# Kernel tuning notes

Hardware: AMD Instinct MI355X
Metric: run time of the kernel (lower is better)

The kernel has to match this reference:

```python
import jax, jax.numpy as jnp
import numpy as np

N_NODES = 50000
N_EDGES = 1600000
D_IN = 128
D_HID = 128
D_OUT = 3
EPS = 1e-5


def setup_inputs() -> dict:
    key = jax.random.key(0)
    ks = jax.random.split(key, 16)
    def lin(k, fi, fo):
        s = 1.0 / np.sqrt(fi)
        return jax.random.uniform(k, (fi, fo), jnp.float32, -s, s)
    inp = {
        "x": jax.random.normal(ks[0], (N_NODES, D_IN), jnp.float32),
        "edge_index": jax.random.randint(ks[1], (2, N_EDGES), 0, N_NODES, jnp.int32),
        "W1": lin(ks[2], D_IN, D_HID), "b1": jnp.zeros((D_HID,), jnp.float32),
        "W2": lin(ks[3], D_HID, D_HID), "b2": jnp.zeros((D_HID,), jnp.float32),
        "W3": lin(ks[4], D_HID, D_HID), "b3": jnp.zeros((D_HID,), jnp.float32),
        "g1": jnp.ones((D_HID,), jnp.float32), "beta1": jnp.zeros((D_HID,), jnp.float32),
        "g2": jnp.ones((D_HID,), jnp.float32), "beta2": jnp.zeros((D_HID,), jnp.float32),
        "Wp1": lin(ks[5], D_HID, D_HID), "bp1": jnp.zeros((D_HID,), jnp.float32),
        "Wp2": lin(ks[6], D_HID, D_OUT), "bp2": jnp.zeros((D_OUT,), jnp.float32),
    }
    return inp


def _gcn_norm(edge_index, n):
    # add self-loops, symmetric normalization (PyG GCNConv default)
    loops = jnp.arange(n, dtype=edge_index.dtype)
    row = jnp.concatenate([edge_index[0], loops])  # source
    col = jnp.concatenate([edge_index[1], loops])  # target
    deg = jax.ops.segment_sum(jnp.ones_like(col, jnp.float32), col, num_segments=n)
    dinv = jnp.where(deg > 0, jax.lax.rsqrt(deg), 0.0)
    norm = dinv[row] * dinv[col]  # [E+N]
    return row, col, norm


def _gcn_conv(x, W, b, row, col, norm, n):
    h = x @ W                                # [N, F]
    msg = h[row] * norm[:, None]             # [E+N, F] gather
    out = jax.ops.segment_sum(msg, col, num_segments=n)  # scatter-add
    return out + b


def _layernorm(x, g, beta):
    mu = jnp.mean(x, axis=-1, keepdims=True)
    var = jnp.var(x, axis=-1, keepdims=True)
    return (x - mu) * jax.lax.rsqrt(var + EPS) * g + beta


def reference(x, edge_index, W1, b1, W2, b2, W3, b3, g1, beta1, g2, beta2, Wp1, bp1, Wp2, bp2):
    n = x.shape[0]
    row, col, norm = _gcn_norm(edge_index, n)
    # layer 0
    h = _gcn_conv(x, W1, b1, row, col, norm, n)
    h = _layernorm(jax.nn.relu(h), g1, beta1)  # dropout = identity (eval mode)
    # layer 1
    h = _gcn_conv(h, W2, b2, row, col, norm, n)
    h = _layernorm(jax.nn.relu(h), g2, beta2)
    # layer 2 (no layernorm)
    h = _gcn_conv(h, W3, b3, row, col, norm, n)
    h = jax.nn.relu(h)
    # post-MP MLP head (dropout = identity in eval)
    h = h @ Wp1 + bp1
    return h @ Wp2 + bp2
```

## Files before the change

kernel.cpp:

```cpp
#include <hip/hip_runtime.h>
#include <hip/hip_bf16.h>

#define EPS_LN 1e-5f
#define NB    256
#define SEGCAP 16384

typedef int ivec4 __attribute__((ext_vector_type(4)));
typedef short bf16x8v __attribute__((ext_vector_type(8)));
typedef float f32x4v __attribute__((ext_vector_type(4)));


__global__ __launch_bounds__(256) void bucket_hist(const int* __restrict__ col,
                                                   int* __restrict__ chunkBH,
                                                   int E, int per, int nbuck) {
    __shared__ int hist[256];
    int t = threadIdx.x;
    hist[t] = 0;
    __syncthreads();
    int s0 = blockIdx.x * per;
    int s1 = s0 + per; if (s1 > E) s1 = E;
    if (s0 < s1) {
        int q0 = s0 >> 2, q1 = s1 >> 2;
        for (int i = q0 + t; i < q1; i += 256) {
            ivec4 c = __builtin_nontemporal_load((const ivec4*)col + i);
            atomicAdd(&hist[c.x >> 8], 1);
            atomicAdd(&hist[c.y >> 8], 1);
            atomicAdd(&hist[c.z >> 8], 1);
            atomicAdd(&hist[c.w >> 8], 1);
        }
        for (int i = (q1 << 2) + t; i < s1; i += 256)
            atomicAdd(&hist[col[i] >> 8], 1);
    }
    __syncthreads();
    if (t < nbuck) chunkBH[blockIdx.x * 256 + t] = hist[t];
}

__global__ __launch_bounds__(256) void bucket_scan(int* __restrict__ chunkBH,
                                                   int* __restrict__ bucketStart,
                                                   int* __restrict__ rowPtr,
                                                   int E, int n, int nbuck, int nb) {
    __shared__ int tot[256];
    int t = threadIdx.x;
    int run = 0;
    if (t < nbuck) {
        for (int k0 = 0; k0 < nb; k0 += 16) {
            int v[16];
#pragma unroll
            for (int j = 0; j < 16; j++)
                v[j] = (k0 + j < nb) ? chunkBH[(k0 + j) * 256 + t] : 0;
#pragma unroll
            for (int j = 0; j < 16; j++) {
                int tv = v[j];
                if (k0 + j < nb) chunkBH[(k0 + j) * 256 + t] = run;
                run += tv;
            }
        }
    }
    tot[t] = run;
    __syncthreads();
    for (int d = 1; d < 256; d <<= 1) {
        int add = (t >= d) ? tot[t - d] : 0;
        __syncthreads();
        tot[t] += add;
        __syncthreads();
    }
    if (t < nbuck) bucketStart[t] = tot[t] - run;
    if (t == 0) { bucketStart[nbuck] = E; rowPtr[n] = E; }
}

__global__ __launch_bounds__(256) void scatter_pairs(const int* __restrict__ row,
                                                     const int* __restrict__ col,
                                                     const int* __restrict__ chunkBH,
                                                     const int* __restrict__ bucketStart,
                                                     unsigned long long* __restrict__ tmp,
                                                     int E, int per, int nbuck) {
    __shared__ int curs[256];
    int t = threadIdx.x;
    int k = blockIdx.x;
    curs[t] = (t < nbuck) ? (chunkBH[k * 256 + t] + bucketStart[t]) : 0;
    __syncthreads();
    int s0 = k * per;
    int s1 = s0 + per; if (s1 > E) s1 = E;
    if (s0 >= s1) return;
    int q0 = s0 >> 2, q1 = s1 >> 2;
    for (int i = q0 + t; i < q1; i += 256) {
        ivec4 c4 = __builtin_nontemporal_load((const ivec4*)col + i);
        ivec4 r4 = __builtin_nontemporal_load((const ivec4*)row + i);
        int p0 = atomicAdd(&curs[c4.x >> 8], 1);
        tmp[p0] = ((unsigned long long)(unsigned)c4.x << 32) | (unsigned)r4.x;
        int p1 = atomicAdd(&curs[c4.y >> 8], 1);
        tmp[p1] = ((unsigned long long)(unsigned)c4.y << 32) | (unsigned)r4.y;
        int p2 = atomicAdd(&curs[c4.z >> 8], 1);
        tmp[p2] = ((unsigned long long)(unsigned)c4.z << 32) | (unsigned)r4.z;
        int p3 = atomicAdd(&curs[c4.w >> 8], 1);
        tmp[p3] = ((unsigned long long)(unsigned)c4.w << 32) | (unsigned)r4.w;
    }
    for (int i = (q1 << 2) + t; i < s1; i += 256) {
        int c = col[i], r = row[i];
        int p = atomicAdd(&curs[c >> 8], 1);
        tmp[p] = ((unsigned long long)(unsigned)c << 32) | (unsigned)r;
    }
}

__global__ __launch_bounds__(256) void bucket_fill(const unsigned long long* __restrict__ tmp,
                                                   const int* __restrict__ bucketStart,
                                                   int* __restrict__ rowPtr,
                                                   float* __restrict__ dinv,
                                                   int* __restrict__ srcList,
                                                   int n) {
    __shared__ int cnt[256];
    __shared__ int cur[256];
    __shared__ int seg[SEGCAP];
    int b = blockIdx.x, t = threadIdx.x;
    int node0 = b << 8;
    int s0 = bucketStart[b], s1 = bucketStart[b + 1];
    int len = s1 - s0;
    cnt[t] = 0;
    __syncthreads();
    for (int i = s0 + t; i < s1; i += 256) {
        int c = (int)(tmp[i] >> 32);
        atomicAdd(&cnt[c - node0], 1);
    }
    __syncthreads();
    int v = cnt[t];
    cur[t] = v;
    __syncthreads();
    for (int d = 1; d < 256; d <<= 1) {
        int add = (t >= d) ? cur[t - d] : 0;
        __syncthreads();
        cur[t] += add;
        __syncthreads();
    }
    int excl = cur[t] - v;
    int node = node0 + t;
    if (node < n) {
        rowPtr[node] = s0 + excl;
        dinv[node] = rsqrtf((float)v + 1.0f);
    }
    cur[t] = excl;
    __syncthreads();
    if (len <= SEGCAP) {
        for (int i = s0 + t; i < s1; i += 256) {
            unsigned long long p = tmp[i];
            int c = (int)(p >> 32);
            int r = (int)(p & 0xffffffffu);
            int pos = atomicAdd(&cur[c - node0], 1);
            seg[pos] = r;
        }
        __syncthreads();
        for (int i = t; i < len; i += 256)
            srcList[s0 + i] = seg[i];
    } else {
        for (int i = s0 + t; i < s1; i += 256) {
            unsigned long long p = tmp[i];
            int c = (int)(p >> 32);
            int r = (int)(p & 0xffffffffu);
            int pos = atomicAdd(&cur[c - node0], 1);
            srcList[s0 + pos] = r;
        }
    }
}

__global__ __launch_bounds__(256) void pack_w(const float* __restrict__ W,
                                              unsigned short* __restrict__ Wp) {
    int t = threadIdx.x;
    for (int s = t; s < 16384; s += 256) {
        int i = s & 7;
        int lane = (s >> 3) & 63;
        int jt = (s >> 9) & 7;
        int kb = s >> 12;
        int k = kb * 32 + ((lane >> 4) & 3) * 8 + i;
        int nn = jt * 16 + (lane & 15);
        float v = W[k * 128 + nn];
        __hip_bfloat16 hi = __float2bfloat16(v);
        float hf = __bfloat162float(hi);
        __hip_bfloat16 lo = __float2bfloat16(v - hf);
        Wp[s]         = *(unsigned short*)&hi;
        Wp[16384 + s] = *(unsigned short*)&lo;
    }
}

__global__ __launch_bounds__(256) void cast_hilo(const float* __restrict__ x,
                                                 unsigned short* __restrict__ hi,
                                                 unsigned short* __restrict__ lo,
                                                 int total4) {
    int i = blockIdx.x * 256 + threadIdx.x;
    if (i >= total4) return;
    float4 v = ((const float4*)x)[i];
    ushort4 h, l;
    __hip_bfloat16 b;
    float f;
    b = __float2bfloat16(v.x); f = __bfloat162float(b); h.x = *(unsigned short*)&b;
    b = __float2bfloat16(v.x - f); l.x = *(unsigned short*)&b;
    b = __float2bfloat16(v.y); f = __bfloat162float(b); h.y = *(unsigned short*)&b;
    b = __float2bfloat16(v.y - f); l.y = *(unsigned short*)&b;
    b = __float2bfloat16(v.z); f = __bfloat162float(b); h.z = *(unsigned short*)&b;
    b = __float2bfloat16(v.z - f); l.z = *(unsigned short*)&b;
    b = __float2bfloat16(v.w); f = __bfloat162float(b); h.w = *(unsigned short*)&b;
    b = __float2bfloat16(v.w - f); l.w = *(unsigned short*)&b;
    ((ushort4*)hi)[i] = h;
    ((ushort4*)lo)[i] = l;
}

__global__ __launch_bounds__(256) void gemm_mfma(const unsigned short* __restrict__ Ahi,
                                                 const unsigned short* __restrict__ Alo,
                                                 const unsigned short* __restrict__ Wp,
                                                 const float* __restrict__ dinv,
                                                 unsigned short* __restrict__ hbOut,
                                                 int n) {
    const int tx = threadIdx.x;
    const int wv = tx >> 6;
    const int l  = tx & 63;
    const int m0 = blockIdx.x * 64 + wv * 16;
    int arow = m0 + (l & 15);
    if (arow >= n) arow = 0;
    const int kofs = (l >> 4) * 8;

    f32x4v acc[8];
#pragma unroll
    for (int jt = 0; jt < 8; jt++) acc[jt] = (f32x4v){0.f, 0.f, 0.f, 0.f};

#pragma unroll
    for (int kb = 0; kb < 4; kb++) {
        bf16x8v ah = *(const bf16x8v*)(Ahi + (size_t)arow * 128 + kb * 32 + kofs);
        bf16x8v al = *(const bf16x8v*)(Alo + (size_t)arow * 128 + kb * 32 + kofs);
        const unsigned short* wb = Wp + (kb * 8) * 512 + l * 8;
#pragma unroll
        for (int jt = 0; jt < 8; jt++) {
            bf16x8v bh = *(const bf16x8v*)(wb + jt * 512);
            bf16x8v bl = *(const bf16x8v*)(wb + jt * 512 + 16384);
            acc[jt] = __builtin_amdgcn_mfma_f32_16x16x32_bf16(ah, bh, acc[jt], 0, 0, 0);
            acc[jt] = __builtin_amdgcn_mfma_f32_16x16x32_bf16(ah, bl, acc[jt], 0, 0, 0);
            acc[jt] = __builtin_amdgcn_mfma_f32_16x16x32_bf16(al, bh, acc[jt], 0, 0, 0);
        }
    }

    const int r0 = m0 + (l >> 4) * 4;
    const int colb = l & 15;
#pragma unroll
    for (int r = 0; r < 4; r++) {
        int grow = r0 + r;
        if (grow < n) {
            float dv = dinv[grow];
#pragma unroll
            for (int jt = 0; jt < 8; jt++) {
                __hip_bfloat16 t = __float2bfloat16(acc[jt][r] * dv);
                hbOut[(size_t)grow * 128 + jt * 16 + colb] = *(unsigned short*)&t;
            }
        }
    }
}

#define BF_LO(u) __uint_as_float((u) << 16)
#define BF_HI(u) __uint_as_float((u) & 0xffff0000u)

__global__ __launch_bounds__(128) void agg_post(const unsigned int* __restrict__ hb,
                                                const int* __restrict__ rowPtr,
                                                const int* __restrict__ srcList,
                                                const float* __restrict__ dinv,
                                                const float* __restrict__ b,
                                                const float* __restrict__ g,
                                                const float* __restrict__ beta,
                                                unsigned short* __restrict__ outHi,
                                                unsigned short* __restrict__ outLo,
                                                int n) {
    int wid = (blockIdx.x * 128 + threadIdx.x) >> 6;
    int lane = threadIdx.x & 63;
    if (wid >= n) return;
    int h = lane & 15;
    int gg = lane >> 4;
    int e0 = rowPtr[wid], e1 = rowPtr[wid + 1];
    float dc = dinv[wid];
    const uint4* hb4 = (const uint4*)hb;

    uint4 us = hb4[(size_t)wid * 16 + h];

    float a[8];
#pragma unroll
    for (int j = 0; j < 8; j++) a[j] = 0.f;

    int idx0 = (e0 + gg < e1) ? srcList[e0 + gg] : -1;
    int idx1 = (e0 + 4 + gg < e1) ? srcList[e0 + 4 + gg] : -1;
    int e = e0;
    for (; e + 8 <= e1; e += 8) {
        int ni0 = (e + 8 + gg < e1) ? srcList[e + 8 + gg] : -1;
        int ni1 = (e + 12 + gg < e1) ? srcList[e + 12 + gg] : -1;
        uint4 u0 = hb4[(size_t)idx0 * 16 + h];
        uint4 u1 = hb4[(size_t)idx1 * 16 + h];
        a[0] += BF_LO(u0.x); a[1] += BF_HI(u0.x);
        a[2] += BF_LO(u0.y); a[3] += BF_HI(u0.y);
        a[4] += BF_LO(u0.z); a[5] += BF_HI(u0.z);
        a[6] += BF_LO(u0.w); a[7] += BF_HI(u0.w);
        a[0] += BF_LO(u1.x); a[1] += BF_HI(u1.x);
        a[2] += BF_LO(u1.y); a[3] += BF_HI(u1.y);
        a[4] += BF_LO(u1.z); a[5] += BF_HI(u1.z);
        a[6] += BF_LO(u1.w); a[7] += BF_HI(u1.w);
        idx0 = ni0; idx1 = ni1;
    }
    if (idx0 >= 0) {
        uint4 u = hb4[(size_t)idx0 * 16 + h];
        a[0] += BF_LO(u.x); a[1] += BF_HI(u.x);
        a[2] += BF_LO(u.y); a[3] += BF_HI(u.y);
        a[4] += BF_LO(u.z); a[5] += BF_HI(u.z);
        a[6] += BF_LO(u.w); a[7] += BF_HI(u.w);
    }
    if (idx1 >= 0) {
        uint4 u = hb4[(size_t)idx1 * 16 + h];
        a[0] += BF_LO(u.x); a[1] += BF_HI(u.x);
        a[2] += BF_LO(u.y); a[3] += BF_HI(u.y);
        a[4] += BF_LO(u.z); a[5] += BF_HI(u.z);
        a[6] += BF_LO(u.w); a[7] += BF_HI(u.w);
    }
#pragma unroll
    for (int j = 0; j < 8; j++) {
        a[j] += __shfl_xor(a[j], 16, 64);
        a[j] += __shfl_xor(a[j], 32, 64);
    }
    a[0] += BF_LO(us.x); a[1] += BF_HI(us.x);
    a[2] += BF_LO(us.y); a[3] += BF_HI(us.y);
    a[4] += BF_LO(us.z); a[5] += BF_HI(us.z);
    a[6] += BF_LO(us.w); a[7] += BF_HI(us.w);

    float4 bv0 = *(const float4*)(b + h * 8);
    float4 bv1 = *(const float4*)(b + h * 8 + 4);
    a[0] = fmaxf(a[0] * dc + bv0.x, 0.f);
    a[1] = fmaxf(a[1] * dc + bv0.y, 0.f);
    a[2] = fmaxf(a[2] * dc + bv0.z, 0.f);
    a[3] = fmaxf(a[3] * dc + bv0.w, 0.f);
    a[4] = fmaxf(a[4] * dc + bv1.x, 0.f);
    a[5] = fmaxf(a[5] * dc + bv1.y, 0.f);
    a[6] = fmaxf(a[6] * dc + bv1.z, 0.f);
    a[7] = fmaxf(a[7] * dc + bv1.w, 0.f);

    float s = ((a[0] + a[1]) + (a[2] + a[3])) + ((a[4] + a[5]) + (a[6] + a[7]));
#pragma unroll
    for (int m = 8; m >= 1; m >>= 1) s += __shfl_xor(s, m, 64);
    float mu = s * (1.f / 128.f);
    float sq = 0.f;
    float d[8];
#pragma unroll
    for (int j = 0; j < 8; j++) { d[j] = a[j] - mu; sq += d[j] * d[j]; }
#pragma unroll
    for (int m = 8; m >= 1; m >>= 1) sq += __shfl_xor(sq, m, 64);
    float rs = rsqrtf(sq * (1.f / 128.f) + EPS_LN);
    float4 gv0 = *(const float4*)(g + h * 8);
    float4 gv1 = *(const float4*)(g + h * 8 + 4);
    float4 bt0 = *(const float4*)(beta + h * 8);
    float4 bt1 = *(const float4*)(beta + h * 8 + 4);
    a[0] = d[0] * rs * gv0.x + bt0.x;
    a[1] = d[1] * rs * gv0.y + bt0.y;
    a[2] = d[2] * rs * gv0.z + bt0.z;
    a[3] = d[3] * rs * gv0.w + bt0.w;
    a[4] = d[4] * rs * gv1.x + bt1.x;
    a[5] = d[5] * rs * gv1.y + bt1.y;
    a[6] = d[6] * rs * gv1.z + bt1.z;
    a[7] = d[7] * rs * gv1.w + bt1.w;

    if (gg == 0) {
        ushort4 h0, h1, l0, l1;
        __hip_bfloat16 bb; float ff;
        bb = __float2bfloat16(a[0]); ff = __bfloat162float(bb); h0.x = *(unsigned short*)&bb;
        bb = __float2bfloat16(a[0] - ff); l0.x = *(unsigned short*)&bb;
        bb = __float2bfloat16(a[1]); ff = __bfloat162float(bb); h0.y = *(unsigned short*)&bb;
        bb = __float2bfloat16(a[1] - ff); l0.y = *(unsigned short*)&bb;
        bb = __float2bfloat16(a[2]); ff = __bfloat162float(bb); h0.z = *(unsigned short*)&bb;
        bb = __float2bfloat16(a[2] - ff); l0.z = *(unsigned short*)&bb;
        bb = __float2bfloat16(a[3]); ff = __bfloat162float(bb); h0.w = *(unsigned short*)&bb;
        bb = __float2bfloat16(a[3] - ff); l0.w = *(unsigned short*)&bb;
        bb = __float2bfloat16(a[4]); ff = __bfloat162float(bb); h1.x = *(unsigned short*)&bb;
        bb = __float2bfloat16(a[4] - ff); l1.x = *(unsigned short*)&bb;
        bb = __float2bfloat16(a[5]); ff = __bfloat162float(bb); h1.y = *(unsigned short*)&bb;
        bb = __float2bfloat16(a[5] - ff); l1.y = *(unsigned short*)&bb;
        bb = __float2bfloat16(a[6]); ff = __bfloat162float(bb); h1.z = *(unsigned short*)&bb;
        bb = __float2bfloat16(a[6] - ff); l1.z = *(unsigned short*)&bb;
        bb = __float2bfloat16(a[7]); ff = __bfloat162float(bb); h1.w = *(unsigned short*)&bb;
        bb = __float2bfloat16(a[7] - ff); l1.w = *(unsigned short*)&bb;
        size_t base = (size_t)wid * 128 + h * 8;
        *(ushort4*)(outHi + base)     = h0;
        *(ushort4*)(outHi + base + 4) = h1;
        *(ushort4*)(outLo + base)     = l0;
        *(ushort4*)(outLo + base + 4) = l1;
    }
}

__global__ __launch_bounds__(128) void agg_head(
        const unsigned int* __restrict__ hb,
        const int* __restrict__ rowPtr,
        const int* __restrict__ srcList,
        const float* __restrict__ dinv,
        const float* __restrict__ b,
        const float* __restrict__ Weff,
        const float* __restrict__ beff,
        float* __restrict__ out, int n) {
    __shared__ float Wl[384];
    int tt = threadIdx.x;
    Wl[tt] = Weff[tt]; Wl[tt + 128] = Weff[tt + 128]; Wl[tt + 256] = Weff[tt + 256];
    __syncthreads();

    int wid = (blockIdx.x * 128 + tt) >> 6;
    int lane = tt & 63;
    if (wid >= n) return;
    int h = lane & 15;
    int gg = lane >> 4;
    int e0 = rowPtr[wid], e1 = rowPtr[wid + 1];
    float dc = dinv[wid];
    const uint4* hb4 = (const uint4*)hb;
    uint4 us = hb4[(size_t)wid * 16 + h];

    float a[8];
#pragma unroll
    for (int j = 0; j < 8; j++) a[j] = 0.f;

    int idx0 = (e0 + gg < e1) ? srcList[e0 + gg] : -1;
    int idx1 = (e0 + 4 + gg < e1) ? srcList[e0 + 4 + gg] : -1;
    int e = e0;
    for (; e + 8 <= e1; e += 8) {
        int ni0 = (e + 8 + gg < e1) ? srcList[e + 8 + gg] : -1;
        int ni1 = (e + 12 + gg < e1) ? srcList[e + 12 + gg] : -1;
        uint4 u0 = hb4[(size_t)idx0 * 16 + h];
        uint4 u1 = hb4[(size_t)idx1 * 16 + h];
        a[0] += BF_LO(u0.x); a[1] += BF_HI(u0.x);
        a[2] += BF_LO(u0.y); a[3] += BF_HI(u0.y);
        a[4] += BF_LO(u0.z); a[5] += BF_HI(u0.z);
        a[6] += BF_LO(u0.w); a[7] += BF_HI(u0.w);
        a[0] += BF_LO(u1.x); a[1] += BF_HI(u1.x);
        a[2] += BF_LO(u1.y); a[3] += BF_HI(u1.y);
        a[4] += BF_LO(u1.z); a[5] += BF_HI(u1.z);
        a[6] += BF_LO(u1.w); a[7] += BF_HI(u1.w);
        idx0 = ni0; idx1 = ni1;
    }
    if (idx0 >= 0) {
        uint4 u = hb4[(size_t)idx0 * 16 + h];
        a[0] += BF_LO(u.x); a[1] += BF_HI(u.x);
        a[2] += BF_LO(u.y); a[3] += BF_HI(u.y);
        a[4] += BF_LO(u.z); a[5] += BF_HI(u.z);
        a[6] += BF_LO(u.w); a[7] += BF_HI(u.w);
    }
    if (idx1 >= 0) {
        uint4 u = hb4[(size_t)idx1 * 16 + h];
        a[0] += BF_LO(u.x); a[1] += BF_HI(u.x);
        a[2] += BF_LO(u.y); a[3] += BF_HI(u.y);
        a[4] += BF_LO(u.z); a[5] += BF_HI(u.z);
        a[6] += BF_LO(u.w); a[7] += BF_HI(u.w);
    }
#pragma unroll
    for (int j = 0; j < 8; j++) {
        a[j] += __shfl_xor(a[j], 16, 64);
        a[j] += __shfl_xor(a[j], 32, 64);
    }
    a[0] += BF_LO(us.x); a[1] += BF_HI(us.x);
    a[2] += BF_LO(us.y); a[3] += BF_HI(us.y);
    a[4] += BF_LO(us.z); a[5] += BF_HI(us.z);
    a[6] += BF_LO(us.w); a[7] += BF_HI(us.w);

    float4 bv0 = *(const float4*)(b + h * 8);
    float4 bv1 = *(const float4*)(b + h * 8 + 4);
    a[0] = fmaxf(a[0] * dc + bv0.x, 0.f);
    a[1] = fmaxf(a[1] * dc + bv0.y, 0.f);
    a[2] = fmaxf(a[2] * dc + bv0.z, 0.f);
    a[3] = fmaxf(a[3] * dc + bv0.w, 0.f);
    a[4] = fmaxf(a[4] * dc + bv1.x, 0.f);
    a[5] = fmaxf(a[5] * dc + bv1.y, 0.f);
    a[6] = fmaxf(a[6] * dc + bv1.z, 0.f);
    a[7] = fmaxf(a[7] * dc + bv1.w, 0.f);

    float p0 = 0.f, p1 = 0.f, p2 = 0.f;
#pragma unroll
    for (int j = 0; j < 8; j++) {
        const float* w = &Wl[(8 * h + j) * 3];
        p0 += a[j] * w[0];
        p1 += a[j] * w[1];
        p2 += a[j] * w[2];
    }
#pragma unroll
    for (int m = 8; m >= 1; m >>= 1) {
        p0 += __shfl_xor(p0, m, 64);
        p1 += __shfl_xor(p1, m, 64);
        p2 += __shfl_xor(p2, m, 64);
    }
    if (lane == 0) {
        out[(size_t)wid * 3 + 0] = p0 + beff[0];
        out[(size_t)wid * 3 + 1] = p1 + beff[1];
        out[(size_t)wid * 3 + 2] = p2 + beff[2];
    }
}

__global__ __launch_bounds__(128) void head_collapse(const float* __restrict__ Wp1,
                                                     const float* __restrict__ bp1,
                                                     const float* __restrict__ Wp2,
                                                     const float* __restrict__ bp2,
                                                     float* __restrict__ Weff,
                                                     float* __restrict__ beff) {
    __shared__ float w2[384];
    int t = threadIdx.x;
    w2[t] = Wp2[t]; w2[t + 128] = Wp2[t + 128]; w2[t + 256] = Wp2[t + 256];
    __syncthreads();
    float p0 = 0.f, p1 = 0.f, p2 = 0.f;
    const float* wr = Wp1 + (size_t)t * 128;
    for (int k = 0; k < 128; k++) {
        float v = wr[k];
        p0 += v * w2[k * 3 + 0];
        p1 += v * w2[k * 3 + 1];
        p2 += v * w2[k * 3 + 2];
    }
    Weff[t * 3 + 0] = p0; Weff[t * 3 + 1] = p1; Weff[t * 3 + 2] = p2;
    if (t == 0) {
        float q0 = bp2[0], q1 = bp2[1], q2 = bp2[2];
        for (int k = 0; k < 128; k++) {
            float v = bp1[k];
            q0 += v * w2[k * 3 + 0];
            q1 += v * w2[k * 3 + 1];
            q2 += v * w2[k * 3 + 2];
        }
        beff[0] = q0; beff[1] = q1; beff[2] = q2;
    }
}

extern "C" void kernel_launch(void* const* d_in, const int* in_sizes, int n_in,
                              void* d_out, int out_size, void* d_ws, size_t ws_size,
                              hipStream_t stream) {
    const float* x   = (const float*)d_in[0];
    const int* ei    = (const int*)d_in[1];
    const float* W1  = (const float*)d_in[2];
    const float* b1  = (const float*)d_in[3];
    const float* W2  = (const float*)d_in[4];
    const float* b2  = (const float*)d_in[5];
    const float* W3  = (const float*)d_in[6];
    const float* b3  = (const float*)d_in[7];
    const float* g1  = (const float*)d_in[8];
    const float* be1 = (const float*)d_in[9];
    const float* g2  = (const float*)d_in[10];
    const float* be2 = (const float*)d_in[11];
    const float* Wp1f = (const float*)d_in[12];
    const float* bp1 = (const float*)d_in[13];
    const float* Wp2f = (const float*)d_in[14];
    const float* bp2 = (const float*)d_in[15];
    float* out = (float*)d_out;

    const int n = in_sizes[0] / 128;
    const int E = in_sizes[1] / 2;
    const int* row = ei;
    const int* col = ei + E;

    char* ws = (char*)d_ws;
    size_t nA  = ((size_t)n * 4 + 255) & ~(size_t)255;
    size_t nA1 = ((size_t)(n + 1) * 4 + 255) & ~(size_t)255;
    size_t eA  = ((size_t)E * 4 + 255) & ~(size_t)255;
    size_t hbSz = ((size_t)n * 128 * 2 + 255) & ~(size_t)255;
    int*   rowPtr  = (int*)ws;
    float* dinvp   = (float*)(ws + nA1);
    int*   srcList = (int*)(ws + nA1 + nA);
    unsigned short* hbA = (unsigned short*)(ws + nA1 + nA + eA);
    unsigned short* hbB = hbA + hbSz / 2;
    unsigned short* Phi = hbB + hbSz / 2;
    unsigned short* Plo = Phi + hbSz / 2;
    unsigned short* Wq1 = Plo + hbSz / 2;
    unsigned short* Wq2 = Wq1 + 32768;
    unsigned short* Wq3 = Wq2 + 32768;
    float* Weff = (float*)(Wq3 + 32768);
    float* beff = Weff + 384;
    unsigned long long* tmp = (unsigned long long*)Phi;
    int* chunkBH     = (int*)((char*)Phi + 2 * eA);
    int* bucketStart = (int*)((char*)Phi + 2 * eA + (size_t)NB * 256 * 4);

    const int nbuck = (n + 255) >> 8;
    const int per   = (((E + NB - 1) / NB) + 15) & ~15;
    const int tileBlocks = (n + 63) / 64;
    const int nodeWaveBlocks = (n + 1) / 2;
    const int castBlocks = (n * 128 / 4 + 255) / 256;

    bucket_hist<<<NB, 256, 0, stream>>>(col, chunkBH, E, per, nbuck);
    bucket_scan<<<1, 256, 0, stream>>>(chunkBH, bucketStart, rowPtr, E, n, nbuck, NB);
    scatter_pairs<<<NB, 256, 0, stream>>>(row, col, chunkBH, bucketStart, tmp, E, per, nbuck);
    bucket_fill<<<nbuck, 256, 0, stream>>>(tmp, bucketStart, rowPtr, dinvp, srcList, n);
    head_collapse<<<1, 128, 0, stream>>>(Wp1f, bp1, Wp2f, bp2, Weff, beff);
    pack_w<<<1, 256, 0, stream>>>(W1, Wq1);
    pack_w<<<1, 256, 0, stream>>>(W2, Wq2);
    pack_w<<<1, 256, 0, stream>>>(W3, Wq3);

    cast_hilo<<<castBlocks, 256, 0, stream>>>(x, Phi, Plo, n * 128 / 4);

    gemm_mfma<<<tileBlocks, 256, 0, stream>>>(Phi, Plo, Wq1, dinvp, hbA, n);
    agg_post<<<nodeWaveBlocks, 128, 0, stream>>>((const unsigned int*)hbA,
                                                 rowPtr, srcList, dinvp,
                                                 b1, g1, be1, Phi, Plo, n);
    gemm_mfma<<<tileBlocks, 256, 0, stream>>>(Phi, Plo, Wq2, dinvp, hbB, n);
    agg_post<<<nodeWaveBlocks, 128, 0, stream>>>((const unsigned int*)hbB,
                                                 rowPtr, srcList, dinvp,
                                                 b2, g2, be2, Phi, Plo, n);
    gemm_mfma<<<tileBlocks, 256, 0, stream>>>(Phi, Plo, Wq3, dinvp, hbA, n);
    agg_head<<<nodeWaveBlocks, 128, 0, stream>>>((const unsigned int*)hbA,
                                                 rowPtr, srcList, dinvp,
                                                 b3, Weff, beff, out, n);
}
```

Before: 414.3 us.

## Fuse input hi/lo split into GEMM, stage weights in LDS, merge weight packing

```diff
diff --git a/kernel.cpp b/kernel.cpp
--- a/kernel.cpp
+++ b/kernel.cpp
@@ -8,6 +8,7 @@
 typedef int ivec4 __attribute__((ext_vector_type(4)));
 typedef short bf16x8v __attribute__((ext_vector_type(8)));
 typedef float f32x4v __attribute__((ext_vector_type(4)));
+typedef unsigned short u16x8 __attribute__((ext_vector_type(8)));
 
 
 __global__ __launch_bounds__(256) void bucket_hist(const int* __restrict__ col,
@@ -161,53 +162,51 @@
     }
 }
 
-__global__ __launch_bounds__(256) void pack_w(const float* __restrict__ W,
-                                              unsigned short* __restrict__ Wp) {
-    int t = threadIdx.x;
-    for (int s = t; s < 16384; s += 256) {
-        int i = s & 7;
-        int lane = (s >> 3) & 63;
-        int jt = (s >> 9) & 7;
-        int kb = s >> 12;
-        int k = kb * 32 + ((lane >> 4) & 3) * 8 + i;
-        int nn = jt * 16 + (lane & 15);
-        float v = W[k * 128 + nn];
-        __hip_bfloat16 hi = __float2bfloat16(v);
-        float hf = __bfloat162float(hi);
-        __hip_bfloat16 lo = __float2bfloat16(v - hf);
-        Wp[s]         = *(unsigned short*)&hi;
-        Wp[16384 + s] = *(unsigned short*)&lo;
-    }
-}
-
-__global__ __launch_bounds__(256) void cast_hilo(const float* __restrict__ x,
-                                                 unsigned short* __restrict__ hi,
-                                                 unsigned short* __restrict__ lo,
-                                                 int total4) {
-    int i = blockIdx.x * 256 + threadIdx.x;
-    if (i >= total4) return;
-    float4 v = ((const float4*)x)[i];
-    ushort4 h, l;
-    __hip_bfloat16 b;
-    float f;
-    b = __float2bfloat16(v.x); f = __bfloat162float(b); h.x = *(unsigned short*)&b;
-    b = __float2bfloat16(v.x - f); l.x = *(unsigned short*)&b;
-    b = __float2bfloat16(v.y); f = __bfloat162float(b); h.y = *(unsigned short*)&b;
-    b = __float2bfloat16(v.y - f); l.y = *(unsigned short*)&b;
-    b = __float2bfloat16(v.z); f = __bfloat162float(b); h.z = *(unsigned short*)&b;
-    b = __float2bfloat16(v.z - f); l.z = *(unsigned short*)&b;
-    b = __float2bfloat16(v.w); f = __bfloat162float(b); h.w = *(unsigned short*)&b;
-    b = __float2bfloat16(v.w - f); l.w = *(unsigned short*)&b;
-    ((ushort4*)hi)[i] = h;
-    ((ushort4*)lo)[i] = l;
-}
-
-__global__ __launch_bounds__(256) void gemm_mfma(const unsigned short* __restrict__ Ahi,
+__global__ __launch_bounds__(256) void pack_w_all(const float* __restrict__ W1,
+                                                  const float* __restrict__ W2,
+                                                  const float* __restrict__ W3,
+                                                  unsigned short* __restrict__ Wq) {
+    int w = blockIdx.x >> 6;
+    const float* W = (w == 0) ? W1 : (w == 1) ? W2 : W3;
+    unsigned short* Wp = Wq + (size_t)w * 32768;
+    int s = (blockIdx.x & 63) * 256 + threadIdx.x;
+    int i = s & 7;
+    int lane = (s >> 3) & 63;
+    int jt = (s >> 9) & 7;
+    int kb = s >> 12;
+    int k = kb * 32 + ((lane >> 4) & 3) * 8 + i;
+    int nn = jt * 16 + (lane & 15);
+    float v = W[k * 128 + nn];
+    __hip_bfloat16 hi = __float2bfloat16(v);
+    float hf = __bfloat162float(hi);
+    __hip_bfloat16 lo = __float2bfloat16(v - hf);
+    Wp[s]         = *(unsigned short*)&hi;
+    Wp[16384 + s] = *(unsigned short*)&lo;
+}
+
+__device__ __forceinline__ void split8(const float* __restrict__ p,
+                                       bf16x8v& ah, bf16x8v& al) {
+#pragma unroll
+    for (int i = 0; i < 8; i++) {
+        float v = p[i];
+        __hip_bfloat16 hb = __float2bfloat16(v);
+        float hf = __bfloat162float(hb);
+        __hip_bfloat16 lb = __float2bfloat16(v - hf);
+        ah[i] = *(short*)&hb;
+        al[i] = *(short*)&lb;
+    }
+}
+
+template<int ASRC>
+__global__ __launch_bounds__(256) void gemm_mfma(const float* __restrict__ Af32,
+                                                 const unsigned short* __restrict__ Ahi,
                                                  const unsigned short* __restrict__ Alo,
                                                  const unsigned short* __restrict__ Wp,
                                                  const float* __restrict__ dinv,
                                                  unsigned short* __restrict__ hbOut,
                                                  int n) {
+    __shared__ unsigned short Bs[8192];
+
     const int tx = threadIdx.x;
     const int wv = tx >> 6;
     const int l  = tx & 63;
@@ -222,13 +221,27 @@
 
 #pragma unroll
     for (int kb = 0; kb < 4; kb++) {
-        bf16x8v ah = *(const bf16x8v*)(Ahi + (size_t)arow * 128 + kb * 32 + kofs);
-        bf16x8v al = *(const bf16x8v*)(Alo + (size_t)arow * 128 + kb * 32 + kofs);
-        const unsigned short* wb = Wp + (kb * 8) * 512 + l * 8;
+        __syncthreads();
+        {
+            u16x8* dH = (u16x8*)&Bs[tx * 16];
+            const u16x8* sH = (const u16x8*)(Wp + kb * 4096 + tx * 16);
+            dH[0] = sH[0]; dH[1] = sH[1];
+            u16x8* dL = (u16x8*)&Bs[4096 + tx * 16];
+            const u16x8* sL = (const u16x8*)(Wp + 16384 + kb * 4096 + tx * 16);
+            dL[0] = sL[0]; dL[1] = sL[1];
+        }
+        bf16x8v ah, al;
+        if (ASRC == 0) {
+            split8(Af32 + (size_t)arow * 128 + kb * 32 + kofs, ah, al);
+        } else {
+            ah = *(const bf16x8v*)(Ahi + (size_t)arow * 128 + kb * 32 + kofs);
+            al = *(const bf16x8v*)(Alo + (size_t)arow * 128 + kb * 32 + kofs);
+        }
+        __syncthreads();
 #pragma unroll
         for (int jt = 0; jt < 8; jt++) {
-            bf16x8v bh = *(const bf16x8v*)(wb + jt * 512);
-            bf16x8v bl = *(const bf16x8v*)(wb + jt * 512 + 16384);
+            bf16x8v bh = *(const bf16x8v*)&Bs[jt * 512 + l * 8];
+            bf16x8v bl = *(const bf16x8v*)&Bs[4096 + jt * 512 + l * 8];
             acc[jt] = __builtin_amdgcn_mfma_f32_16x16x32_bf16(ah, bh, acc[jt], 0, 0, 0);
             acc[jt] = __builtin_amdgcn_mfma_f32_16x16x32_bf16(ah, bl, acc[jt], 0, 0, 0);
             acc[jt] = __builtin_amdgcn_mfma_f32_16x16x32_bf16(al, bh, acc[jt], 0, 0, 0);
@@ -394,7 +407,11 @@
         float* __restrict__ out, int n) {
     __shared__ float Wl[384];
     int tt = threadIdx.x;
-    Wl[tt] = Weff[tt]; Wl[tt + 128] = Weff[tt + 128]; Wl[tt + 256] = Weff[tt + 256];
+    for (int idx = tt; idx < 384; idx += 128) {
+        int f = idx / 3, c = idx - f * 3;
+        int j = f & 7, hh = f >> 3;
+        Wl[(j * 3 + c) * 16 + hh] = Weff[idx];
+    }
     __syncthreads();
 
     int wid = (blockIdx.x * 128 + tt) >> 6;
@@ -467,10 +484,9 @@
     float p0 = 0.f, p1 = 0.f, p2 = 0.f;
 #pragma unroll
     for (int j = 0; j < 8; j++) {
-        const float* w = &Wl[(8 * h + j) * 3];
-        p0 += a[j] * w[0];
-        p1 += a[j] * w[1];
-        p2 += a[j] * w[2];
+        p0 += a[j] * Wl[(j * 3 + 0) * 16 + h];
+        p1 += a[j] * Wl[(j * 3 + 1) * 16 + h];
+        p2 += a[j] * Wl[(j * 3 + 2) * 16 + h];
     }
 #pragma unroll
     for (int m = 8; m >= 1; m >>= 1) {
@@ -554,10 +570,8 @@
     unsigned short* hbB = hbA + hbSz / 2;
     unsigned short* Phi = hbB + hbSz / 2;
     unsigned short* Plo = Phi + hbSz / 2;
-    unsigned short* Wq1 = Plo + hbSz / 2;
-    unsigned short* Wq2 = Wq1 + 32768;
-    unsigned short* Wq3 = Wq2 + 32768;
-    float* Weff = (float*)(Wq3 + 32768);
+    unsigned short* Wq  = Plo + hbSz / 2;
+    float* Weff = (float*)(Wq + 3 * 32768);
     float* beff = Weff + 384;
     unsigned long long* tmp = (unsigned long long*)Phi;
     int* chunkBH     = (int*)((char*)Phi + 2 * eA);
@@ -567,28 +581,23 @@
     const int per   = (((E + NB - 1) / NB) + 15) & ~15;
     const int tileBlocks = (n + 63) / 64;
     const int nodeWaveBlocks = (n + 1) / 2;
-    const int castBlocks = (n * 128 / 4 + 255) / 256;
 
     bucket_hist<<<NB, 256, 0, stream>>>(col, chunkBH, E, per, nbuck);
     bucket_scan<<<1, 256, 0, stream>>>(chunkBH, bucketStart, rowPtr, E, n, nbuck, NB);
     scatter_pairs<<<NB, 256, 0, stream>>>(row, col, chunkBH, bucketStart, tmp, E, per, nbuck);
     bucket_fill<<<nbuck, 256, 0, stream>>>(tmp, bucketStart, rowPtr, dinvp, srcList, n);
     head_collapse<<<1, 128, 0, stream>>>(Wp1f, bp1, Wp2f, bp2, Weff, beff);
-    pack_w<<<1, 256, 0, stream>>>(W1, Wq1);
-    pack_w<<<1, 256, 0, stream>>>(W2, Wq2);
-    pack_w<<<1, 256, 0, stream>>>(W3, Wq3);
-
-    cast_hilo<<<castBlocks, 256, 0, stream>>>(x, Phi, Plo, n * 128 / 4);
-
-    gemm_mfma<<<tileBlocks, 256, 0, stream>>>(Phi, Plo, Wq1, dinvp, hbA, n);
+    pack_w_all<<<192, 256, 0, stream>>>(W1, W2, W3, Wq);
+
+    gemm_mfma<0><<<tileBlocks, 256, 0, stream>>>(x, nullptr, nullptr, Wq, dinvp, hbA, n);
     agg_post<<<nodeWaveBlocks, 128, 0, stream>>>((const unsigned int*)hbA,
                                                  rowPtr, srcList, dinvp,
                                                  b1, g1, be1, Phi, Plo, n);
-    gemm_mfma<<<tileBlocks, 256, 0, stream>>>(Phi, Plo, Wq2, dinvp, hbB, n);
+    gemm_mfma<1><<<tileBlocks, 256, 0, stream>>>(nullptr, Phi, Plo, Wq + 32768, dinvp, hbB, n);
     agg_post<<<nodeWaveBlocks, 128, 0, stream>>>((const unsigned int*)hbB,
                                                  rowPtr, srcList, dinvp,
                                                  b2, g2, be2, Phi, Plo, n);
-    gemm_mfma<<<tileBlocks, 256, 0, stream>>>(Phi, Plo, Wq3, dinvp, hbA, n);
+    gemm_mfma<1><<<tileBlocks, 256, 0, stream>>>(nullptr, Phi, Plo, Wq + 65536, dinvp, hbA, n);
     agg_head<<<nodeWaveBlocks, 128, 0, stream>>>((const unsigned int*)hbA,
                                                  rowPtr, srcList, dinvp,
                                                  b3, Weff, beff, out, n);
```

Result: faster. 364.3 us (-12.1%).
